# Kernel tuning notes

Hardware: AMD Instinct MI355X
Metric: run time of the kernel (lower is better)

The kernel has to match this reference:

```python
import jax, jax.numpy as jnp
import numpy as np
from jax import lax

MIN_TRACK_LEN = 20

def setup_inputs() -> dict:
    key = jax.random.key(0)
    k1, k2 = jax.random.split(key)
    B, F, T, NB = 16, 257, 8000, 64
    mag = jax.random.uniform(k1, (B, F, T), dtype=jnp.float32)          # magnitude spectrogram, >= 0
    freq_fb = jax.random.uniform(k2, (NB, F), dtype=jnp.float32)        # band filterbank
    return {
        "mag": mag,
        "freq_fb": freq_fb,
        "noise_scale": jnp.array(1.5, dtype=jnp.float32),
        "raw_rise": jnp.array(-1.5, dtype=jnp.float32),
        "raw_fall": jnp.array(-3.0, dtype=jnp.float32),
    }

def reference(mag, freq_fb, noise_scale, raw_rise, raw_fall):
    rise = jax.nn.sigmoid(raw_rise)
    fall = jax.nn.sigmoid(raw_fall)
    T = mag.shape[2]
    # initial noise floor from first min_track_len frames: (B, F)
    init_min = jnp.clip(jnp.min(mag[:, :, :min(MIN_TRACK_LEN, T)], axis=2), 1e-5, None)
    floor_min = init_min * 0.5

    def step(noise_floor, frame):  # noise_floor, frame: (B, F)
        alpha = jnp.where(frame > noise_floor, rise, fall)
        nf = (1.0 - alpha) * noise_floor + alpha * frame
        nf = jnp.maximum(nf, floor_min)
        return nf, nf

    _, noise_t = lax.scan(step, init_min, jnp.moveaxis(mag, 2, 0))  # (T, B, F)
    running_noise = jnp.moveaxis(noise_t, 0, 2)                      # (B, F, T)

    vnr = mag / (jnp.abs(noise_scale) * running_noise + 1e-8)        # (B, F, T)
    vnr_bands = jnp.tanh(jnp.einsum('nf,bft->bnt', freq_fb, vnr) / 10.0)
    return jnp.nan_to_num(vnr_bands, nan=0.0, posinf=1.0, neginf=0.0)
```

## Files before the change

### kernel.cpp

```cpp
#include <hip/hip_runtime.h>
#include <stdint.h>

#define B_      16
#define F_      257
#define T_      8000
#define NB_     64
#define TT_     64
#define NTILES  125
#define TPC     2
#define NCHUNK  63
#define WTILES  2
#define LDW     72

typedef __attribute__((ext_vector_type(8))) short short8;
typedef __attribute__((ext_vector_type(4))) float floatx4;

__device__ __forceinline__ unsigned fbits(float x) {
    union { float f; unsigned u; } v; v.f = x; return v.u;
}
__device__ __forceinline__ float ubits(unsigned u) {
    union { float f; unsigned u; } v; v.u = u; return v.f;
}
__device__ __forceinline__ unsigned short f2bf_rne(float x) {
    unsigned u = fbits(x);
    unsigned r = u + 0x7FFFu + ((u >> 16) & 1u);
    return (unsigned short)(r >> 16);
}
__device__ __forceinline__ unsigned packbf(float a, float b) {
    return __builtin_amdgcn_perm(fbits(b), fbits(a), 0x07060302u);
}

__device__ __forceinline__ int stidx(int t, int f) {
    const int st = ((t & 3) << 2) | ((t >> 2) & 3);
    return t * 256 + (f ^ (st << 3));
}


__global__ __launch_bounds__(256, 4) void vnr_fused_kernel(
    const float* __restrict__ mag, const float* __restrict__ fb,
    const float* __restrict__ p_ns, const float* __restrict__ p_rr,
    const float* __restrict__ p_rf, float* __restrict__ out)
{
    __shared__ unsigned short lds[F_ * LDW];
    __shared__ float vnr256s[64];

    const int tid  = threadIdx.x;
    const int lane = tid & 63;
    const int w    = tid >> 6;
    const int l15  = tid & 15;
    const int q    = (tid & 63) >> 4;
    const int fr2  = lane >> 4;
    const int tq   = lane & 15;

    const int bid = blockIdx.x;
    const int b   = bid & 15;
    const int c   = bid >> 4;

    const float ns   = fabsf(p_ns[0]);
    const float rise = 1.0f / (1.0f + __expf(-p_rr[0]));
    const float fall = 1.0f / (1.0f + __expf(-p_rf[0]));

    const float* magp = mag + (size_t)b * (size_t)F_ * (size_t)T_;

    short8 afrag[8];
    {
        const float* fbrow = fb + (16 * w + l15) * F_;
        #pragma unroll
        for (int kt = 0; kt < 8; ++kt) {
            const int f0 = 32 * kt + 8 * q;
            short8 a;
            #pragma unroll
            for (int j = 0; j < 8; ++j) a[j] = (short)f2bf_rne(fbrow[f0 + j]);
            afrag[kt] = a;
        }
    }
    float fb256[4];
    #pragma unroll
    for (int r = 0; r < 4; ++r) fb256[r] = fb[(16 * w + 4 * q + r) * F_ + 256];

    const int f_own = tid;
    float mn = 1e30f;
    #pragma unroll
    for (int t = 0; t < 20; ++t) mn = fminf(mn, magp[(size_t)f_own * T_ + t]);
    const float initv  = fmaxf(mn, 1e-5f);
    const float floorv = 0.5f * initv;
    float nf = initv;

    float nf256 = 0.f, floor256 = 0.f;
    if (tid == 0) {
        float m2 = 1e30f;
        for (int t = 0; t < 20; ++t) m2 = fminf(m2, magp[(size_t)256 * T_ + t]);
        float iv = fmaxf(m2, 1e-5f);
        nf256 = iv; floor256 = 0.5f * iv;
    }

    const int bodyBeg = TPC * c;
    const int tileBeg = (c == 0) ? 0 : max(0, bodyBeg - WTILES);
    const int tileEnd = min(bodyBeg + TPC, NTILES);

    bool prevBody = false;
    for (int tile = tileBeg; tile < tileEnd; ++tile) {
        const bool body = (tile >= bodyBeg);
        const int t0 = tile * TT_;

        if (prevBody) __syncthreads();

        #pragma unroll
        for (int i = 0; i < 16; ++i) {
            const int f = 64 * w + 4 * i + fr2;
            const float4 g = *(const float4*)&magp[(size_t)f * T_ + (t0 + 4 * tq)];
            const unsigned lo = packbf(g.x, g.y);
            const unsigned hi = packbf(g.z, g.w);
            *(uint2*)&lds[LDW * f + 4 * tq] = make_uint2(lo, hi);
        }
        if (tid < 16) {
            const float4 g = *(const float4*)&magp[(size_t)256 * T_ + (t0 + 4 * tid)];
            *(uint2*)&lds[LDW * 256 + 4 * tid] = make_uint2(packbf(g.x, g.y), packbf(g.z, g.w));
        }

        uint4 rv[8];
        #pragma unroll
        for (int j = 0; j < 8; ++j)
            rv[j] = *(const uint4*)&lds[LDW * f_own + 8 * j];

        if (body) __syncthreads();

        {
            float nfl = nf;
            #pragma unroll
            for (int j = 0; j < 64; ++j) {
                const unsigned uu = ((const unsigned*)rv)[j >> 1];
                const float x = ubits((j & 1) ? (uu & 0xFFFF0000u) : (uu << 16));
                const float d = x - nfl;
                const float yr = __builtin_fmaf(rise, d, nfl);
                const float yf = __builtin_fmaf(fall, d, nfl);
                nfl = fmaxf(fmaxf(yr, yf), floorv);
                if (body) {
                    const float vnr = x * __builtin_amdgcn_rcpf(
                                          __builtin_fmaf(ns, nfl, 1e-8f));
                    lds[stidx(j, f_own)] = (unsigned short)(fbits(vnr) >> 16);
                }
            }
            nf = nfl;
        }
        if (tid == 0) {
            float nl = nf256;
            #pragma unroll
            for (int h = 0; h < 2; ++h) {
                uint4 rh[4];
                #pragma unroll
                for (int j = 0; j < 4; ++j)
                    rh[j] = *(const uint4*)&lds[LDW * 256 + 32 * h + 8 * j];
                #pragma unroll
                for (int u = 0; u < 32; ++u) {
                    const unsigned uu = ((const unsigned*)rh)[u >> 1];
                    const float x = ubits((u & 1) ? (uu & 0xFFFF0000u) : (uu << 16));
                    const float d = x - nl;
                    const float yr = __builtin_fmaf(rise, d, nl);
                    const float yf = __builtin_fmaf(fall, d, nl);
                    nl = fmaxf(fmaxf(yr, yf), floor256);
                    if (body) vnr256s[32 * h + u] =
                        x * __builtin_amdgcn_rcpf(__builtin_fmaf(ns, nl, 1e-8f));
                }
            }
            nf256 = nl;
        }

        prevBody = body;
        if (!body) continue;
        __syncthreads();

        const int stl3 = ((((l15 & 3) << 2) | (l15 >> 2)) << 3);
        floatx4 acc[4];
        #pragma unroll
        for (int tt = 0; tt < 4; ++tt) acc[tt] = (floatx4){0.f, 0.f, 0.f, 0.f};
        #pragma unroll
        for (int kt = 0; kt < 8; ++kt) {
            #pragma unroll
            for (int tt = 0; tt < 4; ++tt) {
                const int t = tt * 16 + l15;
                const short8* bp = (const short8*)
                    &lds[t * 256 + ((32 * kt + 8 * q) ^ stl3)];
                acc[tt] = __builtin_amdgcn_mfma_f32_16x16x32_bf16(afrag[kt], *bp, acc[tt], 0, 0, 0);
            }
        }

        const size_t outb = (size_t)b * NB_ * T_;
        #pragma unroll
        for (int tt = 0; tt < 4; ++tt) {
            const int t = tt * 16 + l15;
            const float v256 = vnr256s[t];
            #pragma unroll
            for (int r = 0; r < 4; ++r) {
                const float sv = acc[tt][r] + fb256[r] * v256;
                const float e = __expf(sv * 0.2f);
                const float y = 1.0f - 2.0f * __builtin_amdgcn_rcpf(e + 1.0f);
                out[outb + (size_t)(16 * w + 4 * q + r) * T_ + (size_t)(t0 + t)] = y;
            }
        }
    }
}

extern "C" void kernel_launch(void* const* d_in, const int* in_sizes, int n_in,
                              void* d_out, int out_size, void* d_ws, size_t ws_size,
                              hipStream_t stream) {
    (void)in_sizes; (void)n_in; (void)d_ws; (void)ws_size; (void)out_size;
    const float* mag = (const float*)d_in[0];
    const float* fbp = (const float*)d_in[1];
    const float* nsp = (const float*)d_in[2];
    const float* rr  = (const float*)d_in[3];
    const float* rf  = (const float*)d_in[4];
    float* outp = (float*)d_out;

    dim3 grid(B_ * NCHUNK);
    dim3 block(256);
    hipLaunchKernelGGL(vnr_fused_kernel, grid, block, 0, stream, mag, fbp, nsp, rr, rf, outp);
}
```

Baseline: 254.1 us.

## Software-pipeline mag loads in half-tiles with separate staging and vnr LDS buffers

Splits each 64-frame tile into two 32-frame halves and issues global loads for the next half into registers before scanning the current one, so memory latency overlaps the serial noise-floor recurrence. The LDS is split into a small staging buffer and a dedicated vnr buffer, removing aliasing between the raw-frame staging and the MFMA operand tile. Wave 0 now runs the frequency-256 scan inline alongside its own scan instead of a single-thread tail. Occupancy hint drops from 4 to 3 blocks per CU due to more registers and LDS, and there may be a race if staging is overwritten before all waves finish reading it.

```diff
diff --git a/kernel.cpp b/kernel.cpp
--- a/kernel.cpp
+++ b/kernel.cpp
@@ -10,7 +10,7 @@
 #define TPC     2
 #define NCHUNK  63
 #define WTILES  2
-#define LDW     72
+#define LDSW    40
 
 typedef __attribute__((ext_vector_type(8))) short short8;
 typedef __attribute__((ext_vector_type(4))) float floatx4;
@@ -35,13 +35,63 @@
     return t * 256 + (f ^ (st << 3));
 }
 
-
-__global__ __launch_bounds__(256, 4) void vnr_fused_kernel(
+template<bool BODY, bool DO256>
+static __device__ __forceinline__ void scan_half(
+    unsigned short* __restrict__ vnrR, const unsigned short* __restrict__ stg,
+    float* __restrict__ vnr256s, const int f_own, const int h,
+    float& nf, const float floorv, float& nf256, const float floor256,
+    const float rise, const float fall, const float ns)
+{
+    const int g2    = (f_own >> 3) & 3;
+    const int rbase = LDSW * f_own;
+    uint4 cur = *(const uint4*)&stg[rbase + 8 * (0 ^ g2)];
+    uint4 c256;
+    if (DO256) c256 = *(const uint4*)&stg[LDSW * 256 + 0];
+    float nfl = nf;
+    float nl  = nf256;
+    #pragma unroll
+    for (int c = 0; c < 4; ++c) {
+        uint4 nxt, n256;
+        if (c < 3) {
+            nxt = *(const uint4*)&stg[rbase + 8 * ((c + 1) ^ g2)];
+            if (DO256) n256 = *(const uint4*)&stg[LDSW * 256 + 8 * (c + 1)];
+        }
+        #pragma unroll
+        for (int u = 0; u < 8; ++u) {
+            const int j = h * 32 + c * 8 + u;
+            const unsigned uu = ((const unsigned*)&cur)[u >> 1];
+            const float x = ubits((u & 1) ? (uu & 0xFFFF0000u) : (uu << 16));
+            const float d = x - nfl;
+            nfl = fmaxf(fmaxf(__builtin_fmaf(rise, d, nfl),
+                              __builtin_fmaf(fall, d, nfl)), floorv);
+            if (BODY) {
+                const float vnr = x * __builtin_amdgcn_rcpf(
+                                      __builtin_fmaf(ns, nfl, 1e-8f));
+                vnrR[stidx(j, f_own)] = (unsigned short)(fbits(vnr) >> 16);
+            }
+            if (DO256) {
+                const unsigned vv = ((const unsigned*)&c256)[u >> 1];
+                const float x2 = ubits((u & 1) ? (vv & 0xFFFF0000u) : (vv << 16));
+                const float d2 = x2 - nl;
+                nl = fmaxf(fmaxf(__builtin_fmaf(rise, d2, nl),
+                                 __builtin_fmaf(fall, d2, nl)), floor256);
+                if (BODY) vnr256s[j] = x2 * __builtin_amdgcn_rcpf(
+                                            __builtin_fmaf(ns, nl, 1e-8f));
+            }
+        }
+        if (c < 3) { cur = nxt; if (DO256) c256 = n256; }
+    }
+    nf = nfl;
+    if (DO256) nf256 = nl;
+}
+
+__global__ __launch_bounds__(256, 3) void vnr_fused_kernel(
     const float* __restrict__ mag, const float* __restrict__ fb,
     const float* __restrict__ p_ns, const float* __restrict__ p_rr,
     const float* __restrict__ p_rf, float* __restrict__ out)
 {
-    __shared__ unsigned short lds[F_ * LDW];
+    __shared__ unsigned short vnrR[64 * 256];
+    __shared__ unsigned short stg[F_ * LDSW];
     __shared__ float vnr256s[64];
 
     const int tid  = threadIdx.x;
@@ -49,8 +99,9 @@
     const int w    = tid >> 6;
     const int l15  = tid & 15;
     const int q    = (tid & 63) >> 4;
-    const int fr2  = lane >> 4;
-    const int tq   = lane & 15;
+    const int r8   = lane >> 3;
+    const int s8   = lane & 7;
+    const bool w0  = (w == 0);
 
     const int bid = blockIdx.x;
     const int b   = bid & 15;
@@ -87,10 +138,11 @@
     float nf = initv;
 
     float nf256 = 0.f, floor256 = 0.f;
-    if (tid == 0) {
+    if (w0) {
         float m2 = 1e30f;
+        #pragma unroll
         for (int t = 0; t < 20; ++t) m2 = fminf(m2, magp[(size_t)256 * T_ + t]);
-        float iv = fmaxf(m2, 1e-5f);
+        const float iv = fmaxf(m2, 1e-5f);
         nf256 = iv; floor256 = 0.5f * iv;
     }
 
@@ -98,76 +150,69 @@
     const int tileBeg = (c == 0) ? 0 : max(0, bodyBeg - WTILES);
     const int tileEnd = min(bodyBeg + TPC, NTILES);
 
+    float4 ldv[8];
+    float4 ld256;
+
+    #define ISSUE_HALF(TILE, H)                                               \
+        do {                                                                  \
+            _Pragma("unroll")                                                 \
+            for (int p = 0; p < 8; ++p) {                                     \
+                const int f = 64 * w + 8 * p + r8;                            \
+                ldv[p] = *(const float4*)&magp[(size_t)f * T_ +               \
+                              (TILE) * TT_ + (H) * 32 + 4 * s8];              \
+            }                                                                 \
+            if (w0 && lane < 8)                                               \
+                ld256 = *(const float4*)&magp[(size_t)256 * T_ +              \
+                              (TILE) * TT_ + (H) * 32 + 4 * lane];            \
+        } while (0)
+
+    #define PACK_WRITE()                                                      \
+        do {                                                                  \
+            _Pragma("unroll")                                                 \
+            for (int p = 0; p < 8; ++p) {                                     \
+                const int f   = 64 * w + 8 * p + r8;                          \
+                const int g2f = (8 * w + p) & 3;                              \
+                const int idx = LDSW * f + 8 * ((s8 >> 1) ^ g2f) + 4 * (s8 & 1); \
+                *(uint2*)&stg[idx] = make_uint2(packbf(ldv[p].x, ldv[p].y),   \
+                                                packbf(ldv[p].z, ldv[p].w));  \
+            }                                                                 \
+            if (w0 && lane < 8) {                                             \
+                const int idx = LDSW * 256 + 8 * (lane >> 1) + 4 * (lane & 1);\
+                *(uint2*)&stg[idx] = make_uint2(packbf(ld256.x, ld256.y),     \
+                                                packbf(ld256.z, ld256.w));    \
+            }                                                                 \
+        } while (0)
+
+    #define SCAN(H, BODYF)                                                    \
+        do {                                                                  \
+            if (BODYF) { if (w0) scan_half<true,  true >(vnrR, stg, vnr256s, f_own, H, nf, floorv, nf256, floor256, rise, fall, ns); \
+                         else    scan_half<true,  false>(vnrR, stg, vnr256s, f_own, H, nf, floorv, nf256, floor256, rise, fall, ns); } \
+            else       { if (w0) scan_half<false, true >(vnrR, stg, vnr256s, f_own, H, nf, floorv, nf256, floor256, rise, fall, ns); \
+                         else    scan_half<false, false>(vnrR, stg, vnr256s, f_own, H, nf, floorv, nf256, floor256, rise, fall, ns); } \
+        } while (0)
+
     bool prevBody = false;
+    ISSUE_HALF(tileBeg, 0);
+
     for (int tile = tileBeg; tile < tileEnd; ++tile) {
         const bool body = (tile >= bodyBeg);
         const int t0 = tile * TT_;
 
+        PACK_WRITE();
+        ISSUE_HALF(tile, 1);
         if (prevBody) __syncthreads();
-
-        #pragma unroll
-        for (int i = 0; i < 16; ++i) {
-            const int f = 64 * w + 4 * i + fr2;
-            const float4 g = *(const float4*)&magp[(size_t)f * T_ + (t0 + 4 * tq)];
-            const unsigned lo = packbf(g.x, g.y);
-            const unsigned hi = packbf(g.z, g.w);
-            *(uint2*)&lds[LDW * f + 4 * tq] = make_uint2(lo, hi);
-        }
-        if (tid < 16) {
-            const float4 g = *(const float4*)&magp[(size_t)256 * T_ + (t0 + 4 * tid)];
-            *(uint2*)&lds[LDW * 256 + 4 * tid] = make_uint2(packbf(g.x, g.y), packbf(g.z, g.w));
-        }
-
-        uint4 rv[8];
-        #pragma unroll
-        for (int j = 0; j < 8; ++j)
-            rv[j] = *(const uint4*)&lds[LDW * f_own + 8 * j];
-
-        if (body) __syncthreads();
-
+        SCAN(0, body);
+
+        PACK_WRITE();
         {
-            float nfl = nf;
-            #pragma unroll
-            for (int j = 0; j < 64; ++j) {
-                const unsigned uu = ((const unsigned*)rv)[j >> 1];
-                const float x = ubits((j & 1) ? (uu & 0xFFFF0000u) : (uu << 16));
-                const float d = x - nfl;
-                const float yr = __builtin_fmaf(rise, d, nfl);
-                const float yf = __builtin_fmaf(fall, d, nfl);
-                nfl = fmaxf(fmaxf(yr, yf), floorv);
-                if (body) {
-                    const float vnr = x * __builtin_amdgcn_rcpf(
-                                          __builtin_fmaf(ns, nfl, 1e-8f));
-                    lds[stidx(j, f_own)] = (unsigned short)(fbits(vnr) >> 16);
-                }
-            }
-            nf = nfl;
-        }
-        if (tid == 0) {
-            float nl = nf256;
-            #pragma unroll
-            for (int h = 0; h < 2; ++h) {
-                uint4 rh[4];
-                #pragma unroll
-                for (int j = 0; j < 4; ++j)
-                    rh[j] = *(const uint4*)&lds[LDW * 256 + 32 * h + 8 * j];
-                #pragma unroll
-                for (int u = 0; u < 32; ++u) {
-                    const unsigned uu = ((const unsigned*)rh)[u >> 1];
-                    const float x = ubits((u & 1) ? (uu & 0xFFFF0000u) : (uu << 16));
-                    const float d = x - nl;
-                    const float yr = __builtin_fmaf(rise, d, nl);
-                    const float yf = __builtin_fmaf(fall, d, nl);
-                    nl = fmaxf(fmaxf(yr, yf), floor256);
-                    if (body) vnr256s[32 * h + u] =
-                        x * __builtin_amdgcn_rcpf(__builtin_fmaf(ns, nl, 1e-8f));
-                }
-            }
-            nf256 = nl;
-        }
+            const int tnext = (tile + 1 < tileEnd) ? tile + 1 : tile;
+            ISSUE_HALF(tnext, 0);
+        }
+        SCAN(1, body);
 
         prevBody = body;
         if (!body) continue;
+
         __syncthreads();
 
         const int stl3 = ((((l15 & 3) << 2) | (l15 >> 2)) << 3);
@@ -180,11 +225,10 @@
             for (int tt = 0; tt < 4; ++tt) {
                 const int t = tt * 16 + l15;
                 const short8* bp = (const short8*)
-                    &lds[t * 256 + ((32 * kt + 8 * q) ^ stl3)];
+                    &vnrR[t * 256 + ((32 * kt + 8 * q) ^ stl3)];
                 acc[tt] = __builtin_amdgcn_mfma_f32_16x16x32_bf16(afrag[kt], *bp, acc[tt], 0, 0, 0);
             }
         }
-
         const size_t outb = (size_t)b * NB_ * T_;
         #pragma unroll
         for (int tt = 0; tt < 4; ++tt) {
@@ -193,12 +237,15 @@
             #pragma unroll
             for (int r = 0; r < 4; ++r) {
                 const float sv = acc[tt][r] + fb256[r] * v256;
-                const float e = __expf(sv * 0.2f);
-                const float y = 1.0f - 2.0f * __builtin_amdgcn_rcpf(e + 1.0f);
+                const float e  = __expf(sv * 0.2f);
+                const float y  = 1.0f - 2.0f * __builtin_amdgcn_rcpf(e + 1.0f);
                 out[outb + (size_t)(16 * w + 4 * q + r) * T_ + (size_t)(t0 + t)] = y;
             }
         }
     }
+    #undef ISSUE_HALF
+    #undef PACK_WRITE
+    #undef SCAN
 }
 
 extern "C" void kernel_launch(void* const* d_in, const int* in_sizes, int n_in,
```

Result: no change. 258.7 us (+1.8%).
